# Performance work log

Measured on AMD Instinct MI355X. Metric: run time of the kernel, lower is better.

## Reference

```python
import jax, jax.numpy as jnp
import numpy as np

B, S, D, H = 2, 2048, 1024, 16
DH = D // H
LAMBDA_INIT = 0.8
EPS = 1e-5


def setup_inputs() -> dict:
    key = jax.random.key(0)
    ks = jax.random.split(key, 12)
    inp = {
        "inputs": jax.random.normal(ks[0], (B, S, D), jnp.float32),
        # projection weights stored as [in, out] for right-multiplication
        "wq0": jax.random.normal(ks[1], (D, H * DH), jnp.float32) * 0.02,
        "wq1": jax.random.normal(ks[2], (D, H * DH), jnp.float32) * 0.02,
        "wk0": jax.random.normal(ks[3], (D, H * DH), jnp.float32) * 0.02,
        "wk1": jax.random.normal(ks[4], (D, H * DH), jnp.float32) * 0.02,
        "wv": jax.random.normal(ks[5], (D, H * DH), jnp.float32) * 0.02,
        "wo": jax.random.normal(ks[6], (H * DH, D), jnp.float32) * 0.02,
        # lambda parameter vectors (scaled so exp(dot) stays sane)
        "l0": jax.random.normal(ks[7], (DH,), jnp.float32) * 0.1,
        "l1": jax.random.normal(ks[8], (DH,), jnp.float32) * 0.1,
        "l2": jax.random.normal(ks[9], (DH,), jnp.float32) * 0.1,
        "l3": jax.random.normal(ks[10], (DH,), jnp.float32) * 0.1,
        # per-head LayerNorm params stacked: [H, DH]
        "ln_w": jnp.ones((H, DH), jnp.float32),
        "ln_b": jnp.zeros((H, DH), jnp.float32),
    }
    return inp


def _forward(inputs, wq0, wq1, wk0, wk1, wv, wo, l0, l1, l2, l3, ln_w, ln_b):
    b, s, d = inputs.shape

    def proj(w):  # [b,s,d] @ [d,H*DH] -> [b,H,s,DH]
        return jnp.einsum("bsd,de->bse", inputs, w).reshape(b, s, H, DH).transpose(0, 2, 1, 3)

    q0, q1 = proj(wq0), proj(wq1)
    k0, k1 = proj(wk0), proj(wk1)
    v = proj(wv)

    scale = jax.lax.rsqrt(jnp.float32(DH))
    # ALiBi bias: slope_h * (pos_i - pos_j)
    slopes = (2.0 ** (-8.0 * jnp.arange(1, H + 1, dtype=jnp.float32) / H))  # [H]
    pos = jnp.arange(s, dtype=jnp.float32)
    pos_diff = pos[:, None] - pos[None, :]  # [s,s]
    bias = slopes[None, :, None, None] * pos_diff[None, None, :, :]  # [1,H,s,s]
    causal = jnp.where(jnp.triu(jnp.ones((s, s), bool), 1), -jnp.inf, 0.0)[None, None]

    s0 = jnp.einsum("bhqd,bhkd->bhqk", q0, k0) * scale - bias + causal
    s1 = jnp.einsum("bhqd,bhkd->bhqk", q1, k1) * scale - bias + causal
    w0 = jax.nn.softmax(s0, axis=-1)
    w1 = jax.nn.softmax(s1, axis=-1)

    lamb = (-jnp.exp(jnp.dot(l0, l1)) + LAMBDA_INIT) + (-jnp.exp(jnp.dot(l2, l3)) + LAMBDA_INIT)
    diff_weights = w0 - lamb * w1

    heads = jnp.einsum("bhqk,bhkd->bhqd", diff_weights, v).transpose(0, 2, 1, 3)  # [b,s,H,DH]
    # per-head LayerNorm over DH (biased variance, eps=1e-5)
    mu = jnp.mean(heads, axis=-1, keepdims=True)
    var = jnp.mean((heads - mu) ** 2, axis=-1, keepdims=True)
    normed = (heads - mu) * jax.lax.rsqrt(var + EPS) * ln_w[None, None] + ln_b[None, None]

    attention = normed.reshape(b, s, H * DH)
    return jnp.einsum("bse,ed->bsd", attention, wo)


def reference(inputs, wq0, wq1, wk0, wk1, wv, wo, l0, l1, l2, l3, ln_w, ln_b):
    return _forward(inputs, wq0, wq1, wk0, wk1, wv, wo, l0, l1, l2, l3, ln_w, ln_b)
```

## Files before the change

kernel.cpp:

```cpp
#include <hip/hip_runtime.h>
#include <hip/hip_bf16.h>
#include <math.h>

#define S_LEN   2048
#define NH      16
#define DHEAD   64
#define UMEG    1048576

typedef __attribute__((ext_vector_type(8))) short short8;
typedef __attribute__((ext_vector_type(4))) short short4v;
typedef __attribute__((ext_vector_type(4))) float f32x4;
typedef __attribute__((ext_vector_type(16))) float f32x16;
typedef __attribute__((ext_vector_type(4))) int int4v;

__device__ __forceinline__ f32x4 mfma16(short8 a, short8 b, f32x4 c) {
    return __builtin_amdgcn_mfma_f32_16x16x32_bf16(a, b, c, 0, 0, 0);
}
__device__ __forceinline__ f32x16 mfma32(short8 a, short8 b, f32x16 c) {
    return __builtin_amdgcn_mfma_f32_32x32x16_bf16(a, b, c, 0, 0, 0);
}

__device__ __forceinline__ unsigned short f2bf(float f) {
    unsigned u = __builtin_bit_cast(unsigned, f);
    u = (u + 0x7FFFu + ((u >> 16) & 1u)) >> 16;
    return (unsigned short)u;
}
__device__ __forceinline__ float bf2f(short s) {
    unsigned u = ((unsigned)(unsigned short)s) << 16;
    return __builtin_bit_cast(float, u);
}

__device__ __forceinline__ int cvtpk(float lo, float hi) {
    int w;
    asm("v_cvt_pk_bf16_f32 %0, %1, %2" : "=v"(w) : "v"(lo), "v"(hi));
    return w;
}
__device__ __forceinline__ void pl32swap(int& a, int& b) {
    asm("v_permlane32_swap_b32 %0, %1" : "+v"(a), "+v"(b));
}

#define GLL16(gp, lp) __builtin_amdgcn_global_load_lds( \
    (const __attribute__((address_space(1))) void*)(gp), \
    (__attribute__((address_space(3))) void*)(lp), 16, 0, 0)

__global__ __launch_bounds__(256)
void prep(const float* __restrict__ x, short* __restrict__ xb,
          const float* __restrict__ w0, const float* __restrict__ w1,
          const float* __restrict__ w2, const float* __restrict__ w3,
          const float* __restrict__ w4, const float* __restrict__ w5,
          short* __restrict__ wt)
{
    const int z = blockIdx.z;
    const int tid = threadIdx.x;
    if (z == 6) {
        typedef __attribute__((ext_vector_type(4))) float f4;
        const int bid = blockIdx.y * 16 + blockIdx.x;
        const size_t base = (size_t)bid * 16384 + tid * 4;
#pragma unroll
        for (int i = 0; i < 16; ++i) {
            f4 v = *(const f4*)&x[base + i * 1024];
            short4v o;
            o[0] = (short)f2bf(v[0]); o[1] = (short)f2bf(v[1]);
            o[2] = (short)f2bf(v[2]); o[3] = (short)f2bf(v[3]);
            *(short4v*)&xb[base + i * 1024] = o;
        }
        return;
    }
    __shared__ float t[64][65];
    const float* src = (z == 0) ? w0 : (z == 1) ? w1 : (z == 2) ? w2
                     : (z == 3) ? w3 : (z == 4) ? w4 : w5;
    const float scale = (z <= 1) ? 0.125f * 1.44269504f : 1.0f;
    short* dst = wt + (size_t)z * UMEG;
    const int n0 = blockIdx.x * 64, k0 = blockIdx.y * 64;
    const int c = tid & 63, rb = tid >> 6;
#pragma unroll
    for (int rr = 0; rr < 16; ++rr) {
        const int r = rr * 4 + rb;
        t[r][c] = src[(size_t)(k0 + r) * 1024 + n0 + c];
    }
    __syncthreads();
#pragma unroll
    for (int rr = 0; rr < 16; ++rr) {
        const int n = rr * 4 + rb;
        dst[(size_t)(n0 + n) * 1024 + k0 + c] = (short)f2bf(t[c][n] * scale);
    }
}

__global__ __launch_bounds__(256)
void transp_v(const short* __restrict__ vsrc, short* __restrict__ vdst)
{
    __shared__ short t[64][68];
    const int bh = blockIdx.y;
    const int s0 = blockIdx.x * 64;
    const int tid = threadIdx.x;
    const int c = tid & 63, rb = tid >> 6;
    const size_t base = (size_t)bh * S_LEN * DHEAD;
#pragma unroll
    for (int rr = 0; rr < 16; ++rr) {
        const int r = rr * 4 + rb;
        t[r][c] = vsrc[base + (size_t)(s0 + r) * 64 + c];
    }
    __syncthreads();
#pragma unroll
    for (int rr = 0; rr < 16; ++rr) {
        const int d = rr * 4 + rb;
        vdst[base + (size_t)d * S_LEN + s0 + c] = t[c][d];
    }
}

__global__ __launch_bounds__(256, 2)
void gemm128(const short* __restrict__ A, const short* __restrict__ Wt,
             short* __restrict__ outb, float* __restrict__ outf, int mode)
{
    __shared__ short As[2][128 * 64];
    __shared__ short Bs[2][128 * 64];
    const int tid = threadIdx.x;
    const int l = tid & 63, w = tid >> 6;
    const int wm = w >> 1, wn = w & 1;
    const int lin = (int)blockIdx.x + 8 * (int)blockIdx.y;
    const int xcd = lin & 7, j = lin >> 3;
    const int m0 = (((xcd << 2) | (j >> 3))) * 128;
    const int n0 = (j & 7) * 128;
    const short* Bt = Wt + (size_t)blockIdx.z * UMEG;
    const int srow = l >> 3;
    const int schunk = (l & 7) ^ srow;

    f32x4 acc[4][4];
#pragma unroll
    for (int i = 0; i < 4; ++i)
#pragma unroll
        for (int jj = 0; jj < 4; ++jj)
            acc[i][jj] = (f32x4){0.f, 0.f, 0.f, 0.f};

#define GSTAGE(t_, bi_) do {                                                        \
    _Pragma("unroll")                                                               \
    for (int ii = 0; ii < 4; ++ii) {                                                \
        const int i_ = w * 4 + ii;                                                  \
        GLL16(A  + (size_t)(m0 + 8 * i_ + srow) * 1024 + (t_) * 64 + schunk * 8,    \
              &As[bi_][i_ * 512]);                                                  \
        GLL16(Bt + (size_t)(n0 + 8 * i_ + srow) * 1024 + (t_) * 64 + schunk * 8,    \
              &Bs[bi_][i_ * 512]);                                                  \
    }                                                                               \
} while (0)

    GSTAGE(0, 0);

    for (int t = 0; t < 16; ++t) {
        const int cur = t & 1;
        if (t + 1 < 16) {
            GSTAGE(t + 1, cur ^ 1);
            asm volatile("s_waitcnt vmcnt(8)" ::: "memory");
        } else {
            asm volatile("s_waitcnt vmcnt(0)" ::: "memory");
        }
        __builtin_amdgcn_s_barrier();
#pragma unroll
        for (int kh = 0; kh < 2; ++kh) {
            short8 af[4], bfr[4];
#pragma unroll
            for (int ft = 0; ft < 4; ++ft) {
                const int row = wm * 64 + ft * 16 + (l & 15);
                const int ch = (kh * 4 + (l >> 4)) ^ (row & 7);
                af[ft] = *(const short8*)&As[cur][row * 64 + ch * 8];
            }
#pragma unroll
            for (int nt = 0; nt < 4; ++nt) {
                const int row = wn * 64 + nt * 16 + (l & 15);
                const int ch = (kh * 4 + (l >> 4)) ^ (row & 7);
                bfr[nt] = *(const short8*)&Bs[cur][row * 64 + ch * 8];
            }
            __builtin_amdgcn_s_setprio(1);
#pragma unroll
            for (int i = 0; i < 4; ++i)
#pragma unroll
                for (int jj = 0; jj < 4; ++jj)
                    acc[i][jj] = mfma16(af[i], bfr[jj], acc[i][jj]);
            __builtin_amdgcn_s_setprio(0);
        }
        __builtin_amdgcn_s_barrier();
    }
#undef GSTAGE

    const size_t zoff = (blockIdx.z == 4) ? (size_t)24 * UMEG
                                          : (size_t)blockIdx.z * (4 * UMEG);
#pragma unroll
    for (int i = 0; i < 4; ++i)
#pragma unroll
        for (int jj = 0; jj < 4; ++jj)
#pragma unroll
            for (int r = 0; r < 4; ++r) {
                const int m = m0 + wm * 64 + i * 16 + (l >> 4) * 4 + r;
                const int n = n0 + wn * 64 + jj * 16 + (l & 15);
                const float v = acc[i][jj][r];
                if (mode == 0) {
                    const int b = m >> 11, s = m & 2047;
                    const int h = n >> 6, dh = n & 63;
                    outb[zoff + (((size_t)(b * NH + h)) * S_LEN + s) * DHEAD + dh]
                        = (short)f2bf(v);
                } else {
                    outf[(size_t)m * 1024 + n] = v;
                }
            }
}

__global__ __launch_bounds__(256, 2)
void diff_attn_mfma(const short* __restrict__ pbuf, const short* __restrict__ vtb,
                    short* __restrict__ partO, float* __restrict__ partml)
{
    __shared__ short Ks[3][3][64 * 64];

    const int tid = threadIdx.x;
    const int l = tid & 63, w = tid >> 6;
    const int il = l & 31, hi = l >> 5;
    const int bh = blockIdx.x;
    const int h = bh & 15;
    const int p = blockIdx.y >> 1;
    const int jh = blockIdx.y & 1;
    const int qtA = 15 - p, qtB = p;
    const int szA = qtA + 1, szB = qtB + 1;
    const int ktA0 = jh * szA, ktB0 = jh * szB;

    const size_t MAT = (size_t)4 * UMEG;
    const size_t hoff = (size_t)bh * S_LEN * DHEAD;
    const short* q0g = pbuf + 0 * MAT + hoff;
    const short* q1g = pbuf + 1 * MAT + hoff;
    const short* k0g = pbuf + 2 * MAT + hoff;
    const short* k1g = pbuf + 3 * MAT + hoff;
    const short* vtg = vtb + hoff;

    const float slope2 = exp2f(-0.5f * (float)(h + 1)) * 1.44269504f;

    int qt_cur = qtA;
    int rg = qtA * 128 + w * 32 + il;

    short8 qf0[4], qf1[4];
#pragma unroll
    for (int dblk = 0; dblk < 4; ++dblk) {
        qf0[dblk] = *(const short8*)&q0g[(size_t)rg * 64 + dblk * 16 + hi * 8];
        qf1[dblk] = *(const short8*)&q1g[(size_t)rg * 64 + dblk * 16 + hi * 8];
    }

    f32x16 ot0[2], ot1[2];
#pragma unroll
    for (int mb = 0; mb < 2; ++mb)
#pragma unroll
        for (int r = 0; r < 16; ++r) { ot0[mb][r] = 0.f; ot1[mb][r] = 0.f; }
    float m0r = -100000.f, m1r = -100000.f, l0r = 0.f, l1r = 0.f;

    const int srw = l >> 3;
    const int schunk = (l & 7) ^ srw;

#define KT_OF(s_) (((s_) < szA) ? (ktA0 + (s_)) : (ktB0 + ((s_) - szA)))

#define STAGE(kt_, bi_) do {                                                        \
    _Pragma("unroll")                                                               \
    for (int ii = 0; ii < 2; ++ii) {                                                \
        const int i_ = w * 2 + ii;                                                  \
        GLL16(k0g + (size_t)((kt_) * 64 + 8 * i_ + srw) * 64 + schunk * 8,          \
              &Ks[bi_][0][i_ * 512]);                                               \
        GLL16(k1g + (size_t)((kt_) * 64 + 8 * i_ + srw) * 64 + schunk * 8,          \
              &Ks[bi_][1][i_ * 512]);                                               \
        GLL16(vtg + (size_t)(8 * i_ + srw) * S_LEN + (kt_) * 64 + schunk * 8,       \
              &Ks[bi_][2][i_ * 512]);                                               \
    }                                                                               \
} while (0)

#define SAVEPART(qt_) do {                                                          \
    const int job_ = ((bh << 4) + (qt_)) * 2 + jh;                                  \
    if (hi == 0) {                                                                  \
        float4 mlv;                                                                 \
        mlv.x = m0r; mlv.y = l0r; mlv.z = m1r; mlv.w = l1r;                         \
        *(float4*)&partml[((size_t)job_ * 128 + w * 32 + il) * 4] = mlv;            \
    }                                                                               \
    _Pragma("unroll")                                                               \
    for (int mb_ = 0; mb_ < 2; ++mb_)                                               \
        _Pragma("unroll")                                                           \
        for (int rq_ = 0; rq_ < 4; ++rq_) {                                         \
            union { int wi[2]; short4v sv; } s0u, s1u;                              \
            s0u.wi[0] = cvtpk(ot0[mb_][rq_ * 4 + 0], ot0[mb_][rq_ * 4 + 1]);        \
            s0u.wi[1] = cvtpk(ot0[mb_][rq_ * 4 + 2], ot0[mb_][rq_ * 4 + 3]);        \
            s1u.wi[0] = cvtpk(ot1[mb_][rq_ * 4 + 0], ot1[mb_][rq_ * 4 + 1]);        \
            s1u.wi[1] = cvtpk(ot1[mb_][rq_ * 4 + 2], ot1[mb_][rq_ * 4 + 3]);        \
            const size_t ob_ = (size_t)job_ * 16384 + (size_t)mb_ * 4096            \
                               + rq_ * 1024 + hi * 512 + (w * 32 + il) * 4;         \
            *(short4v*)&partO[ob_] = s0u.sv;                                        \
            *(short4v*)&partO[ob_ + 8192] = s1u.sv;                                 \
        }                                                                           \
} while (0)

    STAGE(KT_OF(0), 0);

    for (int s = 0; s < 17; ++s) {
        if (s + 1 < 17) {
            STAGE(KT_OF(s + 1), (s + 1) % 3);
            asm volatile("s_waitcnt vmcnt(6)" ::: "memory");
        } else {
            asm volatile("s_waitcnt vmcnt(0)" ::: "memory");
        }
        __builtin_amdgcn_s_barrier();

        const int cur = s % 3;
        const int kt = KT_OF(s);
        const int qw0 = qt_cur * 128 + w * 32;
        if (kt * 64 <= qw0 + 31) {
            f32x16 s0[2], s1[2];
            const float cb0 = slope2 * (float)(kt * 64 + 4 * hi - rg) - m0r;
            const float dm = m0r - m1r;
#pragma unroll
            for (int kvb = 0; kvb < 2; ++kvb) {
                const float cb = cb0 + slope2 * (float)(kvb * 32);
#pragma unroll
                for (int r = 0; r < 16; ++r) {
                    const float pat = (float)((r & 3) + 8 * (r >> 2));
                    s0[kvb][r] = fmaf(slope2, pat, cb);
                    s1[kvb][r] = s0[kvb][r] + dm;
                }
            }

            __builtin_amdgcn_s_setprio(1);
#pragma unroll
            for (int dblk = 0; dblk < 4; ++dblk)
#pragma unroll
                for (int kvb = 0; kvb < 2; ++kvb) {
                    const int rowA = kvb * 32 + il;
                    const int ch = (dblk * 2 + hi) ^ (rowA & 7);
                    const short8 k0f = *(const short8*)&Ks[cur][0][rowA * 64 + ch * 8];
                    const short8 k1f = *(const short8*)&Ks[cur][1][rowA * 64 + ch * 8];
                    s0[kvb] = mfma32(k0f, qf0[dblk], s0[kvb]);
                    s1[kvb] = mfma32(k1f, qf1[dblk], s1[kvb]);
                }
            __builtin_amdgcn_s_setprio(0);

            if (kt * 64 + 63 > qw0) {
                const int mth = rg - kt * 64;
#pragma unroll
                for (int kvb = 0; kvb < 2; ++kvb)
#pragma unroll
                    for (int r = 0; r < 16; ++r) {
                        const int kvoff = kvb * 32 + (r & 3) + 8 * (r >> 2) + 4 * hi;
                        if (kvoff > mth) { s0[kvb][r] = -1e30f; s1[kvb][r] = -1e30f; }
                    }
            }

            float t0[8], t1[8];
#pragma unroll
            for (int r = 0; r < 8; ++r) {
                t0[r] = fmaxf(fmaxf(s0[0][r], s0[0][r + 8]), fmaxf(s0[1][r], s0[1][r + 8]));
                t1[r] = fmaxf(fmaxf(s1[0][r], s1[0][r + 8]), fmaxf(s1[1][r], s1[1][r + 8]));
            }
            float pm0 = fmaxf(fmaxf(fmaxf(t0[0], t0[1]), fmaxf(t0[2], t0[3])),
                              fmaxf(fmaxf(t0[4], t0[5]), fmaxf(t0[6], t0[7])));
            float pm1 = fmaxf(fmaxf(fmaxf(t1[0], t1[1]), fmaxf(t1[2], t1[3])),
                              fmaxf(fmaxf(t1[4], t1[5]), fmaxf(t1[6], t1[7])));
            pm0 = fmaxf(pm0, __shfl_xor(pm0, 32));
            pm1 = fmaxf(pm1, __shfl_xor(pm1, 32));

            if (__any(pm0 > 8.f || pm1 > 8.f)) {
                const float d0 = fmaxf(pm0, 0.f), d1 = fmaxf(pm1, 0.f);
                const float sc0 = __builtin_amdgcn_exp2f(-d0);
                const float sc1 = __builtin_amdgcn_exp2f(-d1);
#pragma unroll
                for (int mb = 0; mb < 2; ++mb)
#pragma unroll
                    for (int r = 0; r < 16; ++r) {
                        ot0[mb][r] *= sc0;
                        ot1[mb][r] *= sc1;
                    }
                l0r *= sc0; l1r *= sc1;
                m0r += d0; m1r += d1;
#pragma unroll
                for (int kvb = 0; kvb < 2; ++kvb)
#pragma unroll
                    for (int r = 0; r < 16; ++r) {
                        s0[kvb][r] -= d0;
                        s1[kvb][r] -= d1;
                    }
            }

#pragma unroll
            for (int kvb = 0; kvb < 2; ++kvb)
#pragma unroll
                for (int r = 0; r < 16; ++r) {
                    s0[kvb][r] = __builtin_amdgcn_exp2f(s0[kvb][r]);
                    s1[kvb][r] = __builtin_amdgcn_exp2f(s1[kvb][r]);
                }
            float u0[8], u1[8];
#pragma unroll
            for (int r = 0; r < 8; ++r) {
                u0[r] = (s0[0][r] + s0[0][r + 8]) + (s0[1][r] + s0[1][r + 8]);
                u1[r] = (s1[0][r] + s1[0][r + 8]) + (s1[1][r] + s1[1][r + 8]);
            }
            float rs0 = ((u0[0] + u0[1]) + (u0[2] + u0[3])) + ((u0[4] + u0[5]) + (u0[6] + u0[7]));
            float rs1 = ((u1[0] + u1[1]) + (u1[2] + u1[3])) + ((u1[4] + u1[5]) + (u1[6] + u1[7]));
            rs0 += __shfl_xor(rs0, 32);
            rs1 += __shfl_xor(rs1, 32);
            l0r += rs0; l1r += rs1;

            short8 pa0[4], pa1[4];
#pragma unroll
            for (int ks = 0; ks < 4; ++ks) {
                const int kvb = ks >> 1, rb = (ks & 1) * 8;
                int wa0 = cvtpk(s0[kvb][rb + 0], s0[kvb][rb + 1]);
                int wb0 = cvtpk(s0[kvb][rb + 2], s0[kvb][rb + 3]);
                int wc0 = cvtpk(s0[kvb][rb + 4], s0[kvb][rb + 5]);
                int wd0 = cvtpk(s0[kvb][rb + 6], s0[kvb][rb + 7]);
                pl32swap(wa0, wc0);
                pl32swap(wb0, wd0);
                int wa1 = cvtpk(s1[kvb][rb + 0], s1[kvb][rb + 1]);
                int wb1 = cvtpk(s1[kvb][rb + 2], s1[kvb][rb + 3]);
                int wc1 = cvtpk(s1[kvb][rb + 4], s1[kvb][rb + 5]);
                int wd1 = cvtpk(s1[kvb][rb + 6], s1[kvb][rb + 7]);
                pl32swap(wa1, wc1);
                pl32swap(wb1, wd1);
                union { int4v wi; short8 sv; } u0u, u1u;
                u0u.wi[0] = wa0; u0u.wi[1] = wb0; u0u.wi[2] = wc0; u0u.wi[3] = wd0;
                u1u.wi[0] = wa1; u1u.wi[1] = wb1; u1u.wi[2] = wc1; u1u.wi[3] = wd1;
                pa0[ks] = u0u.sv;
                pa1[ks] = u1u.sv;
            }

            __builtin_amdgcn_s_setprio(1);
#pragma unroll
            for (int mb = 0; mb < 2; ++mb)
#pragma unroll
                for (int ks = 0; ks < 4; ++ks) {
                    const int rowV = mb * 32 + il;
                    const int ch = (ks * 2 + hi) ^ (rowV & 7);
                    const short8 vf = *(const short8*)&Ks[cur][2][rowV * 64 + ch * 8];
                    ot0[mb] = mfma32(vf, pa0[ks], ot0[mb]);
                    ot1[mb] = mfma32(vf, pa1[ks], ot1[mb]);
                }
            __builtin_amdgcn_s_setprio(0);
        }

        if (s == szA - 1) {
            SAVEPART(qtA);
#pragma unroll
            for (int mb = 0; mb < 2; ++mb)
#pragma unroll
                for (int r = 0; r < 16; ++r) { ot0[mb][r] = 0.f; ot1[mb][r] = 0.f; }
            m0r = -100000.f; m1r = -100000.f; l0r = 0.f; l1r = 0.f;
            qt_cur = qtB;
            rg = qtB * 128 + w * 32 + il;
#pragma unroll
            for (int dblk = 0; dblk < 4; ++dblk) {
                qf0[dblk] = *(const short8*)&q0g[(size_t)rg * 64 + dblk * 16 + hi * 8];
                qf1[dblk] = *(const short8*)&q1g[(size_t)rg * 64 + dblk * 16 + hi * 8];
            }
        }
    }
    SAVEPART(qtB);
#undef SAVEPART
#undef STAGE
#undef KT_OF
}

__global__ __launch_bounds__(256)
void merge_ln(const short* __restrict__ partO, const float* __restrict__ partml,
              const float* __restrict__ l0v, const float* __restrict__ l1v,
              const float* __restrict__ l2v, const float* __restrict__ l3v,
              const float* __restrict__ lnw, const float* __restrict__ lnb,
              short* __restrict__ atb)
{
    const int t = threadIdx.x;
    const int bh = blockIdx.y, b = bh >> 4, h = bh & 15;
    const int rl = t >> 2;
    const int srow = blockIdx.x * 64 + rl;
    const int qt = srow >> 7, rit = srow & 127;
    const int sub = t & 3, mb = sub >> 1, hs = sub & 1;

    float d01 = 0.f, d23 = 0.f;
    for (int i = 0; i < 64; ++i) { d01 += l0v[i] * l1v[i]; d23 += l2v[i] * l3v[i]; }
    const float lamb = (-__expf(d01) + 0.8f) + (-__expf(d23) + 0.8f);

    const size_t jA = ((size_t)(bh * 16 + qt)) * 2;
    const float4 mlA = *(const float4*)&partml[(jA * 128 + rit) * 4];
    const float4 mlB = *(const float4*)&partml[((jA + 1) * 128 + rit) * 4];
    const float mm0 = fmaxf(mlA.x, mlB.x);
    const float sA0 = exp2f(mlA.x - mm0), sB0 = exp2f(mlB.x - mm0);
    const float lc0 = mlA.y * sA0 + mlB.y * sB0;
    const float mm1 = fmaxf(mlA.z, mlB.z);
    const float sA1 = exp2f(mlA.z - mm1), sB1 = exp2f(mlB.z - mm1);
    const float lc1 = mlA.w * sA1 + mlB.w * sB1;
    const float i0 = 1.f / lc0, i1 = 1.f / lc1;

    float hv[16];
#pragma unroll
    for (int rq = 0; rq < 4; ++rq) {
        const size_t ob = jA * 16384 + (size_t)mb * 4096 + rq * 1024 + hs * 512 + rit * 4;
        const short4v a0 = *(const short4v*)&partO[ob];
        const short4v a1 = *(const short4v*)&partO[ob + 8192];
        const short4v b0 = *(const short4v*)&partO[ob + 16384];
        const short4v b1 = *(const short4v*)&partO[ob + 16384 + 8192];
#pragma unroll
        for (int jx = 0; jx < 4; ++jx) {
            const float v0 = (bf2f(a0[jx]) * sA0 + bf2f(b0[jx]) * sB0) * i0;
            const float v1 = (bf2f(a1[jx]) * sA1 + bf2f(b1[jx]) * sB1) * i1;
            hv[rq * 4 + jx] = v0 - lamb * v1;
        }
    }

    float s = 0.f;
#pragma unroll
    for (int r = 0; r < 16; ++r) s += hv[r];
    s += __shfl_xor(s, 1); s += __shfl_xor(s, 2);
    const float mu = s * (1.f / 64.f);
    float vs = 0.f;
#pragma unroll
    for (int r = 0; r < 16; ++r) { const float dd = hv[r] - mu; vs += dd * dd; }
    vs += __shfl_xor(vs, 1); vs += __shfl_xor(vs, 2);
    const float rstd = rsqrtf(vs * (1.f / 64.f) + 1e-5f);

    short* orow = atb + ((size_t)(b * S_LEN + srow)) * 1024 + h * 64;
#pragma unroll
    for (int rq = 0; rq < 4; ++rq) {
        const int d0 = mb * 32 + rq * 8 + hs * 4;
        float o[4];
#pragma unroll
        for (int jx = 0; jx < 4; ++jx)
            o[jx] = (hv[rq * 4 + jx] - mu) * rstd * lnw[h * 64 + d0 + jx] + lnb[h * 64 + d0 + jx];
        union { int wi[2]; short4v sv; } st;
        st.wi[0] = cvtpk(o[0], o[1]);
        st.wi[1] = cvtpk(o[2], o[3]);
        *(short4v*)&orow[d0] = st.sv;
    }
}

extern "C" void kernel_launch(void* const* d_in, const int* in_sizes, int n_in,
                              void* d_out, int out_size, void* d_ws, size_t ws_size,
                              hipStream_t stream)
{
    (void)in_sizes; (void)n_in; (void)out_size; (void)ws_size;
    const float* x   = (const float*)d_in[0];
    const float* wq0 = (const float*)d_in[1];
    const float* wq1 = (const float*)d_in[2];
    const float* wk0 = (const float*)d_in[3];
    const float* wk1 = (const float*)d_in[4];
    const float* wv  = (const float*)d_in[5];
    const float* wo  = (const float*)d_in[6];
    const float* l0  = (const float*)d_in[7];
    const float* l1  = (const float*)d_in[8];
    const float* l2  = (const float*)d_in[9];
    const float* l3  = (const float*)d_in[10];
    const float* lnw = (const float*)d_in[11];
    const float* lnb = (const float*)d_in[12];
    float* out = (float*)d_out;
    short* ws = (short*)d_ws;

    short* wtcat  = ws;
    short* qk     = ws + (size_t)6  * UMEG;
    short* vtb    = ws + (size_t)22 * UMEG;
    short* atb    = ws + (size_t)26 * UMEG;
    short* xb     = atb;
    short* partO  = ws + (size_t)30 * UMEG;
    short* vorig  = partO;
    float* partml = (float*)(ws + (size_t)46 * UMEG);

    prep<<<dim3(16, 16, 7), 256, 0, stream>>>(x, xb, wq0, wq1, wk0, wk1, wv, wo, wtcat);
    gemm128<<<dim3(8, 32, 5), 256, 0, stream>>>(xb, wtcat, qk, nullptr, 0);
    transp_v<<<dim3(32, 32), 256, 0, stream>>>(vorig, vtb);
    diff_attn_mfma<<<dim3(32, 16), 256, 0, stream>>>(qk, vtb, partO, partml);
    merge_ln<<<dim3(32, 32), 256, 0, stream>>>(partO, partml,
                                               l0, l1, l2, l3, lnw, lnb, atb);
    gemm128<<<dim3(8, 32, 1), 256, 0, stream>>>(atb, wtcat + (size_t)5 * UMEG,
                                                nullptr, out, 1);
}
```

Baseline: 175.7 us.

## Software-pipeline attention loop: overlap QK/softmax of next tile with PV of current

```diff
diff --git a/kernel.cpp b/kernel.cpp
--- a/kernel.cpp
+++ b/kernel.cpp
@@ -247,6 +247,8 @@
         for (int r = 0; r < 16; ++r) { ot0[mb][r] = 0.f; ot1[mb][r] = 0.f; }
     float m0r = -100000.f, m1r = -100000.f, l0r = 0.f, l1r = 0.f;
 
+    short8 pa0[4], pa1[4];
+
     const int srw = l >> 3;
     const int schunk = (l & 7) ^ srw;
 
@@ -288,152 +290,156 @@
         }                                                                           \
 } while (0)
 
+#define QKSM(kt_, bi_) do {                                                         \
+    const int qw0_ = qt_cur * 128 + w * 32;                                         \
+    if ((kt_) * 64 <= qw0_ + 31) {                                                  \
+        f32x16 s0[2], s1[2];                                                        \
+        const float cb0 = slope2 * (float)((kt_) * 64 + 4 * hi - rg) - m0r;         \
+        const float dm = m0r - m1r;                                                 \
+        _Pragma("unroll")                                                           \
+        for (int kvb = 0; kvb < 2; ++kvb) {                                         \
+            const float cb = cb0 + slope2 * (float)(kvb * 32);                      \
+            _Pragma("unroll")                                                       \
+            for (int r = 0; r < 16; ++r) {                                          \
+                const float pat = (float)((r & 3) + 8 * (r >> 2));                  \
+                s0[kvb][r] = fmaf(slope2, pat, cb);                                 \
+                s1[kvb][r] = s0[kvb][r] + dm;                                       \
+            }                                                                       \
+        }                                                                           \
+        __builtin_amdgcn_s_setprio(1);                                              \
+        _Pragma("unroll")                                                           \
+        for (int dblk = 0; dblk < 4; ++dblk)                                        \
+            _Pragma("unroll")                                                       \
+            for (int kvb = 0; kvb < 2; ++kvb) {                                     \
+                const int rowA = kvb * 32 + il;                                     \
+                const int ch = (dblk * 2 + hi) ^ (rowA & 7);                        \
+                const short8 k0f = *(const short8*)&Ks[bi_][0][rowA * 64 + ch * 8]; \
+                const short8 k1f = *(const short8*)&Ks[bi_][1][rowA * 64 + ch * 8]; \
+                s0[kvb] = mfma32(k0f, qf0[dblk], s0[kvb]);                          \
+                s1[kvb] = mfma32(k1f, qf1[dblk], s1[kvb]);                          \
+            }                                                                       \
+        __builtin_amdgcn_s_setprio(0);                                              \
+        if ((kt_) * 64 + 63 > qw0_) {                                               \
+            const int mth = rg - (kt_) * 64;                                        \
+            _Pragma("unroll")                                                       \
+            for (int kvb = 0; kvb < 2; ++kvb)                                       \
+                _Pragma("unroll")                                                   \
+                for (int r = 0; r < 16; ++r) {                                      \
+                    const int kvoff = kvb * 32 + (r & 3) + 8 * (r >> 2) + 4 * hi;   \
+                    if (kvoff > mth) { s0[kvb][r] = -1e30f; s1[kvb][r] = -1e30f; }  \
+                }                                                                   \
+        }                                                                           \
+        float t0[8], t1[8];                                                         \
+        _Pragma("unroll")                                                           \
+        for (int r = 0; r < 8; ++r) {                                               \
+            t0[r] = fmaxf(fmaxf(s0[0][r], s0[0][r + 8]),                            \
+                          fmaxf(s0[1][r], s0[1][r + 8]));                           \
+            t1[r] = fmaxf(fmaxf(s1[0][r], s1[0][r + 8]),                            \
+                          fmaxf(s1[1][r], s1[1][r + 8]));                           \
+        }                                                                           \
+        float pm0 = fmaxf(fmaxf(fmaxf(t0[0], t0[1]), fmaxf(t0[2], t0[3])),          \
+                          fmaxf(fmaxf(t0[4], t0[5]), fmaxf(t0[6], t0[7])));         \
+        float pm1 = fmaxf(fmaxf(fmaxf(t1[0], t1[1]), fmaxf(t1[2], t1[3])),          \
+                          fmaxf(fmaxf(t1[4], t1[5]), fmaxf(t1[6], t1[7])));         \
+        pm0 = fmaxf(pm0, __shfl_xor(pm0, 32));                                      \
+        pm1 = fmaxf(pm1, __shfl_xor(pm1, 32));                                      \
+        if (__any(pm0 > 8.f || pm1 > 8.f)) {                                        \
+            const float d0 = fmaxf(pm0, 0.f), d1 = fmaxf(pm1, 0.f);                 \
+            const float sc0 = __builtin_amdgcn_exp2f(-d0);                          \
+            const float sc1 = __builtin_amdgcn_exp2f(-d1);                          \
+            _Pragma("unroll")                                                       \
+            for (int mb = 0; mb < 2; ++mb)                                          \
+                _Pragma("unroll")                                                   \
+                for (int r = 0; r < 16; ++r) {                                      \
+                    ot0[mb][r] *= sc0;                                              \
+                    ot1[mb][r] *= sc1;                                              \
+                }                                                                   \
+            l0r *= sc0; l1r *= sc1;                                                 \
+            m0r += d0; m1r += d1;                                                   \
+            _Pragma("unroll")                                                       \
+            for (int kvb = 0; kvb < 2; ++kvb)                                       \
+                _Pragma("unroll")                                                   \
+                for (int r = 0; r < 16; ++r) {                                      \
+                    s0[kvb][r] -= d0;                                               \
+                    s1[kvb][r] -= d1;                                               \
+                }                                                                   \
+        }                                                                           \
+        _Pragma("unroll")                                                           \
+        for (int kvb = 0; kvb < 2; ++kvb)                                           \
+            _Pragma("unroll")                                                       \
+            for (int r = 0; r < 16; ++r) {                                          \
+                s0[kvb][r] = __builtin_amdgcn_exp2f(s0[kvb][r]);                    \
+                s1[kvb][r] = __builtin_amdgcn_exp2f(s1[kvb][r]);                    \
+            }                                                                       \
+        float u0[8], u1[8];                                                         \
+        _Pragma("unroll")                                                           \
+        for (int r = 0; r < 8; ++r) {                                               \
+            u0[r] = (s0[0][r] + s0[0][r + 8]) + (s0[1][r] + s0[1][r + 8]);          \
+            u1[r] = (s1[0][r] + s1[0][r + 8]) + (s1[1][r] + s1[1][r + 8]);          \
+        }                                                                           \
+        float rs0 = ((u0[0] + u0[1]) + (u0[2] + u0[3]))                             \
+                  + ((u0[4] + u0[5]) + (u0[6] + u0[7]));                            \
+        float rs1 = ((u1[0] + u1[1]) + (u1[2] + u1[3]))                             \
+                  + ((u1[4] + u1[5]) + (u1[6] + u1[7]));                            \
+        rs0 += __shfl_xor(rs0, 32);                                                 \
+        rs1 += __shfl_xor(rs1, 32);                                                 \
+        l0r += rs0; l1r += rs1;                                                     \
+        _Pragma("unroll")                                                           \
+        for (int ks = 0; ks < 4; ++ks) {                                            \
+            const int kvb = ks >> 1, rb = (ks & 1) * 8;                             \
+            int wa0 = cvtpk(s0[kvb][rb + 0], s0[kvb][rb + 1]);                      \
+            int wb0 = cvtpk(s0[kvb][rb + 2], s0[kvb][rb + 3]);                      \
+            int wc0 = cvtpk(s0[kvb][rb + 4], s0[kvb][rb + 5]);                      \
+            int wd0 = cvtpk(s0[kvb][rb + 6], s0[kvb][rb + 7]);                      \
+            pl32swap(wa0, wc0);                                                     \
+            pl32swap(wb0, wd0);                                                     \
+            int wa1 = cvtpk(s1[kvb][rb + 0], s1[kvb][rb + 1]);                      \
+            int wb1 = cvtpk(s1[kvb][rb + 2], s1[kvb][rb + 3]);                      \
+            int wc1 = cvtpk(s1[kvb][rb + 4], s1[kvb][rb + 5]);                      \
+            int wd1 = cvtpk(s1[kvb][rb + 6], s1[kvb][rb + 7]);                      \
+            pl32swap(wa1, wc1);                                                     \
+            pl32swap(wb1, wd1);                                                     \
+            union { int4v wi; short8 sv; } u0u, u1u;                                \
+            u0u.wi[0] = wa0; u0u.wi[1] = wb0; u0u.wi[2] = wc0; u0u.wi[3] = wd0;     \
+            u1u.wi[0] = wa1; u1u.wi[1] = wb1; u1u.wi[2] = wc1; u1u.wi[3] = wd1;     \
+            pa0[ks] = u0u.sv;                                                       \
+            pa1[ks] = u1u.sv;                                                       \
+        }                                                                           \
+    }                                                                               \
+} while (0)
+
+#define PVST(kt_, bi_) do {                                                         \
+    const int qw0_ = qt_cur * 128 + w * 32;                                         \
+    if ((kt_) * 64 <= qw0_ + 31) {                                                  \
+        __builtin_amdgcn_s_setprio(1);                                              \
+        _Pragma("unroll")                                                           \
+        for (int mb = 0; mb < 2; ++mb)                                              \
+            _Pragma("unroll")                                                       \
+            for (int ks = 0; ks < 4; ++ks) {                                        \
+                const int rowV = mb * 32 + il;                                      \
+                const int ch = (ks * 2 + hi) ^ (rowV & 7);                          \
+                const short8 vf = *(const short8*)&Ks[bi_][2][rowV * 64 + ch * 8];  \
+                ot0[mb] = mfma32(vf, pa0[ks], ot0[mb]);                             \
+                ot1[mb] = mfma32(vf, pa1[ks], ot1[mb]);                             \
+            }                                                                       \
+        __builtin_amdgcn_s_setprio(0);                                              \
+    }                                                                               \
+} while (0)
+
     STAGE(KT_OF(0), 0);
+    STAGE(KT_OF(1), 1);
+    asm volatile("s_waitcnt vmcnt(6)" ::: "memory");
+    __builtin_amdgcn_s_barrier();
+    QKSM(KT_OF(0), 0);
 
     for (int s = 0; s < 17; ++s) {
-        if (s + 1 < 17) {
-            STAGE(KT_OF(s + 1), (s + 1) % 3);
-            asm volatile("s_waitcnt vmcnt(6)" ::: "memory");
-        } else {
-            asm volatile("s_waitcnt vmcnt(0)" ::: "memory");
-        }
+        if (s + 2 <= 16) STAGE(KT_OF(s + 2), (s + 2) % 3);
+        PVST(KT_OF(s), s % 3);
+        if (s == 16) break;
+        if (s + 2 <= 16) asm volatile("s_waitcnt vmcnt(6)" ::: "memory");
+        else             asm volatile("s_waitcnt vmcnt(0)" ::: "memory");
         __builtin_amdgcn_s_barrier();
-
-        const int cur = s % 3;
-        const int kt = KT_OF(s);
-        const int qw0 = qt_cur * 128 + w * 32;
-        if (kt * 64 <= qw0 + 31) {
-            f32x16 s0[2], s1[2];
-            const float cb0 = slope2 * (float)(kt * 64 + 4 * hi - rg) - m0r;
-            const float dm = m0r - m1r;
-#pragma unroll
-            for (int kvb = 0; kvb < 2; ++kvb) {
-                const float cb = cb0 + slope2 * (float)(kvb * 32);
-#pragma unroll
-                for (int r = 0; r < 16; ++r) {
-                    const float pat = (float)((r & 3) + 8 * (r >> 2));
-                    s0[kvb][r] = fmaf(slope2, pat, cb);
-                    s1[kvb][r] = s0[kvb][r] + dm;
-                }
-            }
-
-            __builtin_amdgcn_s_setprio(1);
-#pragma unroll
-            for (int dblk = 0; dblk < 4; ++dblk)
-#pragma unroll
-                for (int kvb = 0; kvb < 2; ++kvb) {
-                    const int rowA = kvb * 32 + il;
-                    const int ch = (dblk * 2 + hi) ^ (rowA & 7);
-                    const short8 k0f = *(const short8*)&Ks[cur][0][rowA * 64 + ch * 8];
-                    const short8 k1f = *(const short8*)&Ks[cur][1][rowA * 64 + ch * 8];
-                    s0[kvb] = mfma32(k0f, qf0[dblk], s0[kvb]);
-                    s1[kvb] = mfma32(k1f, qf1[dblk], s1[kvb]);
-                }
-            __builtin_amdgcn_s_setprio(0);
-
-            if (kt * 64 + 63 > qw0) {
-                const int mth = rg - kt * 64;
-#pragma unroll
-                for (int kvb = 0; kvb < 2; ++kvb)
-#pragma unroll
-                    for (int r = 0; r < 16; ++r) {
-                        const int kvoff = kvb * 32 + (r & 3) + 8 * (r >> 2) + 4 * hi;
-                        if (kvoff > mth) { s0[kvb][r] = -1e30f; s1[kvb][r] = -1e30f; }
-                    }
-            }
-
-            float t0[8], t1[8];
-#pragma unroll
-            for (int r = 0; r < 8; ++r) {
-                t0[r] = fmaxf(fmaxf(s0[0][r], s0[0][r + 8]), fmaxf(s0[1][r], s0[1][r + 8]));
-                t1[r] = fmaxf(fmaxf(s1[0][r], s1[0][r + 8]), fmaxf(s1[1][r], s1[1][r + 8]));
-            }
-            float pm0 = fmaxf(fmaxf(fmaxf(t0[0], t0[1]), fmaxf(t0[2], t0[3])),
-                              fmaxf(fmaxf(t0[4], t0[5]), fmaxf(t0[6], t0[7])));
-            float pm1 = fmaxf(fmaxf(fmaxf(t1[0], t1[1]), fmaxf(t1[2], t1[3])),
-                              fmaxf(fmaxf(t1[4], t1[5]), fmaxf(t1[6], t1[7])));
-            pm0 = fmaxf(pm0, __shfl_xor(pm0, 32));
-            pm1 = fmaxf(pm1, __shfl_xor(pm1, 32));
-
-            if (__any(pm0 > 8.f || pm1 > 8.f)) {
-                const float d0 = fmaxf(pm0, 0.f), d1 = fmaxf(pm1, 0.f);
-                const float sc0 = __builtin_amdgcn_exp2f(-d0);
-                const float sc1 = __builtin_amdgcn_exp2f(-d1);
-#pragma unroll
-                for (int mb = 0; mb < 2; ++mb)
-#pragma unroll
-                    for (int r = 0; r < 16; ++r) {
-                        ot0[mb][r] *= sc0;
-                        ot1[mb][r] *= sc1;
-                    }
-                l0r *= sc0; l1r *= sc1;
-                m0r += d0; m1r += d1;
-#pragma unroll
-                for (int kvb = 0; kvb < 2; ++kvb)
-#pragma unroll
-                    for (int r = 0; r < 16; ++r) {
-                        s0[kvb][r] -= d0;
-                        s1[kvb][r] -= d1;
-                    }
-            }
-
-#pragma unroll
-            for (int kvb = 0; kvb < 2; ++kvb)
-#pragma unroll
-                for (int r = 0; r < 16; ++r) {
-                    s0[kvb][r] = __builtin_amdgcn_exp2f(s0[kvb][r]);
-                    s1[kvb][r] = __builtin_amdgcn_exp2f(s1[kvb][r]);
-                }
-            float u0[8], u1[8];
-#pragma unroll
-            for (int r = 0; r < 8; ++r) {
-                u0[r] = (s0[0][r] + s0[0][r + 8]) + (s0[1][r] + s0[1][r + 8]);
-                u1[r] = (s1[0][r] + s1[0][r + 8]) + (s1[1][r] + s1[1][r + 8]);
-            }
-            float rs0 = ((u0[0] + u0[1]) + (u0[2] + u0[3])) + ((u0[4] + u0[5]) + (u0[6] + u0[7]));
-            float rs1 = ((u1[0] + u1[1]) + (u1[2] + u1[3])) + ((u1[4] + u1[5]) + (u1[6] + u1[7]));
-            rs0 += __shfl_xor(rs0, 32);
-            rs1 += __shfl_xor(rs1, 32);
-            l0r += rs0; l1r += rs1;
-
-            short8 pa0[4], pa1[4];
-#pragma unroll
-            for (int ks = 0; ks < 4; ++ks) {
-                const int kvb = ks >> 1, rb = (ks & 1) * 8;
-                int wa0 = cvtpk(s0[kvb][rb + 0], s0[kvb][rb + 1]);
-                int wb0 = cvtpk(s0[kvb][rb + 2], s0[kvb][rb + 3]);
-                int wc0 = cvtpk(s0[kvb][rb + 4], s0[kvb][rb + 5]);
-                int wd0 = cvtpk(s0[kvb][rb + 6], s0[kvb][rb + 7]);
-                pl32swap(wa0, wc0);
-                pl32swap(wb0, wd0);
-                int wa1 = cvtpk(s1[kvb][rb + 0], s1[kvb][rb + 1]);
-                int wb1 = cvtpk(s1[kvb][rb + 2], s1[kvb][rb + 3]);
-                int wc1 = cvtpk(s1[kvb][rb + 4], s1[kvb][rb + 5]);
-                int wd1 = cvtpk(s1[kvb][rb + 6], s1[kvb][rb + 7]);
-                pl32swap(wa1, wc1);
-                pl32swap(wb1, wd1);
-                union { int4v wi; short8 sv; } u0u, u1u;
-                u0u.wi[0] = wa0; u0u.wi[1] = wb0; u0u.wi[2] = wc0; u0u.wi[3] = wd0;
-                u1u.wi[0] = wa1; u1u.wi[1] = wb1; u1u.wi[2] = wc1; u1u.wi[3] = wd1;
-                pa0[ks] = u0u.sv;
-                pa1[ks] = u1u.sv;
-            }
-
-            __builtin_amdgcn_s_setprio(1);
-#pragma unroll
-            for (int mb = 0; mb < 2; ++mb)
-#pragma unroll
-                for (int ks = 0; ks < 4; ++ks) {
-                    const int rowV = mb * 32 + il;
-                    const int ch = (ks * 2 + hi) ^ (rowV & 7);
-                    const short8 vf = *(const short8*)&Ks[cur][2][rowV * 64 + ch * 8];
-                    ot0[mb] = mfma32(vf, pa0[ks], ot0[mb]);
-                    ot1[mb] = mfma32(vf, pa1[ks], ot1[mb]);
-                }
-            __builtin_amdgcn_s_setprio(0);
-        }
-
-        if (s == szA - 1) {
+        if (s + 1 == szA) {
             SAVEPART(qtA);
 #pragma unroll
             for (int mb = 0; mb < 2; ++mb)
@@ -448,8 +454,11 @@
                 qf1[dblk] = *(const short8*)&q1g[(size_t)rg * 64 + dblk * 16 + hi * 8];
             }
         }
+        QKSM(KT_OF(s + 1), (s + 1) % 3);
     }
     SAVEPART(qtB);
+#undef PVST
+#undef QKSM
 #undef SAVEPART
 #undef STAGE
 #undef KT_OF
```

Result: slower. 216.9 us (+23.4%).

## Generalize attention KV split to three partitions with double-buffered LDS staging

Applied to the files above, without the earlier changes.

```diff
diff --git a/kernel.cpp b/kernel.cpp
--- a/kernel.cpp
+++ b/kernel.cpp
@@ -207,18 +207,23 @@
 void diff_attn_mfma(const short* __restrict__ pbuf, const short* __restrict__ vtb,
                     short* __restrict__ partO, float* __restrict__ partml)
 {
-    __shared__ short Ks[3][3][64 * 64];
+    __shared__ short Ks[2][3][64 * 64];
 
     const int tid = threadIdx.x;
     const int l = tid & 63, w = tid >> 6;
     const int il = l & 31, hi = l >> 5;
     const int bh = blockIdx.x;
     const int h = bh & 15;
-    const int p = blockIdx.y >> 1;
-    const int jh = blockIdx.y & 1;
+    const int NS = (int)gridDim.y >> 3;
+    const int p = (int)blockIdx.y / NS;
+    const int jh = (int)blockIdx.y % NS;
     const int qtA = 15 - p, qtB = p;
     const int szA = qtA + 1, szB = qtB + 1;
-    const int ktA0 = jh * szA, ktB0 = jh * szB;
+    const int rA0 = (2 * szA * jh) / NS;
+    const int nA = (2 * szA * (jh + 1)) / NS - rA0;
+    const int rB0 = (2 * szB * jh) / NS;
+    const int nB = (2 * szB * (jh + 1)) / NS - rB0;
+    const int nsteps = nA + nB;
 
     const size_t MAT = (size_t)4 * UMEG;
     const size_t hoff = (size_t)bh * S_LEN * DHEAD;
@@ -250,7 +255,7 @@
     const int srw = l >> 3;
     const int schunk = (l & 7) ^ srw;
 
-#define KT_OF(s_) (((s_) < szA) ? (ktA0 + (s_)) : (ktB0 + ((s_) - szA)))
+#define KT_OF(g_) (((g_) < nA) ? (rA0 + (g_)) : (rB0 + (g_) - nA))
 
 #define STAGE(kt_, bi_) do {                                                        \
     _Pragma("unroll")                                                               \
@@ -266,7 +271,7 @@
 } while (0)
 
 #define SAVEPART(qt_) do {                                                          \
-    const int job_ = ((bh << 4) + (qt_)) * 2 + jh;                                  \
+    const int job_ = ((bh << 4) + (qt_)) * NS + jh;                                 \
     if (hi == 0) {                                                                  \
         float4 mlv;                                                                 \
         mlv.x = m0r; mlv.y = l0r; mlv.z = m1r; mlv.w = l1r;                         \
@@ -290,17 +295,17 @@
 
     STAGE(KT_OF(0), 0);
 
-    for (int s = 0; s < 17; ++s) {
-        if (s + 1 < 17) {
-            STAGE(KT_OF(s + 1), (s + 1) % 3);
+    for (int g = 0; g < nsteps; ++g) {
+        const int cur = g & 1;
+        if (g + 1 < nsteps) {
+            STAGE(KT_OF(g + 1), cur ^ 1);
             asm volatile("s_waitcnt vmcnt(6)" ::: "memory");
         } else {
             asm volatile("s_waitcnt vmcnt(0)" ::: "memory");
         }
         __builtin_amdgcn_s_barrier();
 
-        const int cur = s % 3;
-        const int kt = KT_OF(s);
+        const int kt = KT_OF(g);
         const int qw0 = qt_cur * 128 + w * 32;
         if (kt * 64 <= qw0 + 31) {
             f32x16 s0[2], s1[2];
@@ -433,7 +438,7 @@
             __builtin_amdgcn_s_setprio(0);
         }
 
-        if (s == szA - 1) {
+        if (g == nA - 1) {
             SAVEPART(qtA);
 #pragma unroll
             for (int mb = 0; mb < 2; ++mb)
@@ -448,6 +453,7 @@
                 qf1[dblk] = *(const short8*)&q1g[(size_t)rg * 64 + dblk * 16 + hi * 8];
             }
         }
+        __builtin_amdgcn_s_barrier();
     }
     SAVEPART(qtB);
 #undef SAVEPART
@@ -460,7 +466,7 @@
               const float* __restrict__ l0v, const float* __restrict__ l1v,
               const float* __restrict__ l2v, const float* __restrict__ l3v,
               const float* __restrict__ lnw, const float* __restrict__ lnb,
-              short* __restrict__ atb)
+              short* __restrict__ atb, int NS)
 {
     const int t = threadIdx.x;
     const int bh = blockIdx.y, b = bh >> 4, h = bh & 15;
@@ -473,18 +479,23 @@
     for (int i = 0; i < 64; ++i) { d01 += l0v[i] * l1v[i]; d23 += l2v[i] * l3v[i]; }
     const float lamb = (-__expf(d01) + 0.8f) + (-__expf(d23) + 0.8f);
 
-    const size_t jA = ((size_t)(bh * 16 + qt)) * 2;
+    const size_t jA = ((size_t)(bh * 16 + qt)) * NS;
     const float4 mlA = *(const float4*)&partml[(jA * 128 + rit) * 4];
     const float4 mlB = *(const float4*)&partml[((jA + 1) * 128 + rit) * 4];
-    const float mm0 = fmaxf(mlA.x, mlB.x);
-    const float sA0 = exp2f(mlA.x - mm0), sB0 = exp2f(mlB.x - mm0);
-    const float lc0 = mlA.y * sA0 + mlB.y * sB0;
-    const float mm1 = fmaxf(mlA.z, mlB.z);
-    const float sA1 = exp2f(mlA.z - mm1), sB1 = exp2f(mlB.z - mm1);
-    const float lc1 = mlA.w * sA1 + mlB.w * sB1;
+    float4 mlC;
+    if (NS == 3) mlC = *(const float4*)&partml[((jA + 2) * 128 + rit) * 4];
+    else { mlC.x = -1e30f; mlC.y = 0.f; mlC.z = -1e30f; mlC.w = 0.f; }
+
+    const float mm0 = fmaxf(fmaxf(mlA.x, mlB.x), mlC.x);
+    const float wA0 = exp2f(mlA.x - mm0), wB0 = exp2f(mlB.x - mm0), wC0 = exp2f(mlC.x - mm0);
+    const float lc0 = mlA.y * wA0 + mlB.y * wB0 + mlC.y * wC0;
+    const float mm1 = fmaxf(fmaxf(mlA.z, mlB.z), mlC.z);
+    const float wA1 = exp2f(mlA.z - mm1), wB1 = exp2f(mlB.z - mm1), wC1 = exp2f(mlC.z - mm1);
+    const float lc1 = mlA.w * wA1 + mlB.w * wB1 + mlC.w * wC1;
     const float i0 = 1.f / lc0, i1 = 1.f / lc1;
 
     float hv[16];
+    const short4v zero4 = (short4v){0, 0, 0, 0};
 #pragma unroll
     for (int rq = 0; rq < 4; ++rq) {
         const size_t ob = jA * 16384 + (size_t)mb * 4096 + rq * 1024 + hs * 512 + rit * 4;
@@ -492,10 +503,12 @@
         const short4v a1 = *(const short4v*)&partO[ob + 8192];
         const short4v b0 = *(const short4v*)&partO[ob + 16384];
         const short4v b1 = *(const short4v*)&partO[ob + 16384 + 8192];
+        const short4v c0 = (NS == 3) ? *(const short4v*)&partO[ob + 32768] : zero4;
+        const short4v c1 = (NS == 3) ? *(const short4v*)&partO[ob + 32768 + 8192] : zero4;
 #pragma unroll
         for (int jx = 0; jx < 4; ++jx) {
-            const float v0 = (bf2f(a0[jx]) * sA0 + bf2f(b0[jx]) * sB0) * i0;
-            const float v1 = (bf2f(a1[jx]) * sA1 + bf2f(b1[jx]) * sB1) * i1;
+            const float v0 = (bf2f(a0[jx]) * wA0 + bf2f(b0[jx]) * wB0 + bf2f(c0[jx]) * wC0) * i0;
+            const float v1 = (bf2f(a1[jx]) * wA1 + bf2f(b1[jx]) * wB1 + bf2f(c1[jx]) * wC1) * i1;
             hv[rq * 4 + jx] = v0 - lamb * v1;
         }
     }
@@ -530,7 +543,7 @@
                               void* d_out, int out_size, void* d_ws, size_t ws_size,
                               hipStream_t stream)
 {
-    (void)in_sizes; (void)n_in; (void)out_size; (void)ws_size;
+    (void)in_sizes; (void)n_in; (void)out_size;
     const float* x   = (const float*)d_in[0];
     const float* wq0 = (const float*)d_in[1];
     const float* wq1 = (const float*)d_in[2];
@@ -547,6 +560,8 @@
     float* out = (float*)d_out;
     short* ws = (short*)d_ws;
 
+    const int NS = (ws_size >= (size_t)56 * UMEG * 2) ? 3 : 2;
+
     short* wtcat  = ws;
     short* qk     = ws + (size_t)6  * UMEG;
     short* vtb    = ws + (size_t)22 * UMEG;
@@ -554,14 +569,14 @@
     short* xb     = atb;
     short* partO  = ws + (size_t)30 * UMEG;
     short* vorig  = partO;
-    float* partml = (float*)(ws + (size_t)46 * UMEG);
+    float* partml = (float*)(ws + (size_t)(30 + 8 * NS) * UMEG);
 
     prep<<<dim3(16, 16, 7), 256, 0, stream>>>(x, xb, wq0, wq1, wk0, wk1, wv, wo, wtcat);
     gemm128<<<dim3(8, 32, 5), 256, 0, stream>>>(xb, wtcat, qk, nullptr, 0);
     transp_v<<<dim3(32, 32), 256, 0, stream>>>(vorig, vtb);
-    diff_attn_mfma<<<dim3(32, 16), 256, 0, stream>>>(qk, vtb, partO, partml);
+    diff_attn_mfma<<<dim3(32, 8 * NS), 256, 0, stream>>>(qk, vtb, partO, partml);
     merge_ln<<<dim3(32, 32), 256, 0, stream>>>(partO, partml,
-                                               l0, l1, l2, l3, lnw, lnb, atb);
+                                               l0, l1, l2, l3, lnw, lnb, atb, NS);
     gemm128<<<dim3(8, 32, 1), 256, 0, stream>>>(atb, wtcat + (size_t)5 * UMEG,
                                                 nullptr, out, 1);
 }
```

After: 183.0 us. +4.1%, slower.
